# Kernel optimization log

Measured on AMD Instinct MI355X. Metric: run time of the kernel, lower is better.

The kernel has to match this reference:

```python
import jax, jax.numpy as jnp
import numpy as np

H = 12          # num_attention_heads
DH = 64         # attention_head_size (768/12)
LDH = 16        # layout head size (DH / channel_shrink_ratio=4)


def _split_heads(x, h, d):
    # [B,S,h*d] -> [B,h,S,d]
    B, S, _ = x.shape
    return x.reshape(B, S, h, d).transpose(0, 2, 1, 3)


def setup_inputs() -> dict:
    key = jax.random.key(0)
    ks = jax.random.split(key, 16)
    B, S, D, LD = 4, 2048, 768, 192
    std = 0.02
    inp = {
        "hidden_states": jax.random.normal(ks[0], (B, S, D), jnp.float32),
        "layout_hidden_states": jax.random.normal(ks[1], (B, S, LD), jnp.float32),
        "attention_mask": jnp.zeros((B, 1, 1, S), jnp.float32),
        # text-stream QKV (weights stored [in, out] so y = x @ W + b)
        "Wq": jax.random.normal(ks[2], (D, D), jnp.float32) * std,
        "bq": jnp.zeros((D,), jnp.float32),
        "Wk": jax.random.normal(ks[3], (D, D), jnp.float32) * std,
        "bk": jnp.zeros((D,), jnp.float32),
        "Wv": jax.random.normal(ks[4], (D, D), jnp.float32) * std,
        "bv": jnp.zeros((D,), jnp.float32),
        # layout-stream QKV
        "LWq": jax.random.normal(ks[5], (LD, LD), jnp.float32) * std,
        "Lbq": jnp.zeros((LD,), jnp.float32),
        "LWk": jax.random.normal(ks[6], (LD, LD), jnp.float32) * std,
        "Lbk": jnp.zeros((LD,), jnp.float32),
        "LWv": jax.random.normal(ks[7], (LD, LD), jnp.float32) * std,
        "Lbv": jnp.zeros((LD,), jnp.float32),
    }
    return inp


def reference(hidden_states, layout_hidden_states, attention_mask,
              Wq, bq, Wk, bk, Wv, bv, LWq, Lbq, LWk, Lbk, LWv, Lbv):
    B, S, D = hidden_states.shape
    LD = layout_hidden_states.shape[-1]

    q = _split_heads(hidden_states @ Wq + bq, H, DH)   # [B,H,S,DH]
    k = _split_heads(hidden_states @ Wk + bk, H, DH)
    v = _split_heads(hidden_states @ Wv + bv, H, DH)
    lq = _split_heads(layout_hidden_states @ LWq + Lbq, H, LDH)  # [B,H,S,LDH]
    lk = _split_heads(layout_hidden_states @ LWk + Lbk, H, LDH)
    lv = _split_heads(layout_hidden_states @ LWv + Lbv, H, LDH)

    # scaled per-stream scores
    scores_t = jnp.einsum('bhqd,bhkd->bhqk', q, k) / np.sqrt(DH).astype(np.float32)
    scores_l = jnp.einsum('bhqd,bhkd->bhqk', lq, lk) / np.sqrt(LDH).astype(np.float32)

    # bidirectional cross-addition (BiACM); layout branch detaches the text scores
    scores_text = scores_t + scores_l + attention_mask
    scores_layout = jax.lax.stop_gradient(scores_t) + scores_l + attention_mask

    probs_t = jax.nn.softmax(scores_text, axis=-1)
    probs_l = jax.nn.softmax(scores_layout, axis=-1)

    ctx = jnp.einsum('bhqk,bhkd->bhqd', probs_t, v)
    ctx = ctx.transpose(0, 2, 1, 3).reshape(B, S, H * DH)       # [B,S,768]
    lctx = jnp.einsum('bhqk,bhkd->bhqd', probs_l, lv)
    lctx = lctx.transpose(0, 2, 1, 3).reshape(B, S, H * LDH)    # [B,S,192]
    return (ctx, lctx)
```

## Files before the change

### kernel.cpp

```cpp
#include <hip/hip_runtime.h>
#include <hip/hip_bf16.h>
#include <cstdint>

typedef __attribute__((ext_vector_type(8))) short bf16x8;
typedef __attribute__((ext_vector_type(4))) float f32x4;

#define MFMA16(a, b, c) __builtin_amdgcn_mfma_f32_16x16x32_bf16((a), (b), (c), 0, 0, 0)

static __device__ __forceinline__ unsigned short f2b(float x) {
  __hip_bfloat16 h = __float2bfloat16(x);
  return __builtin_bit_cast(unsigned short, h);
}

__global__ __launch_bounds__(256) void cvt_f32_bf16(const float* __restrict__ s,
                                                    __hip_bfloat16* __restrict__ d, int n) {
  int stride = gridDim.x * 256 * 4;
  for (int i = (blockIdx.x * 256 + threadIdx.x) * 4; i < n; i += stride) {
    float4 v = *(const float4*)(s + i);
    ushort4 o;
    o.x = f2b(v.x); o.y = f2b(v.y); o.z = f2b(v.z); o.w = f2b(v.w);
    *(ushort4*)&d[i] = o;
  }
}

__global__ __launch_bounds__(256) void transpose_cvt(const float* __restrict__ s0,
                                                     const float* __restrict__ s1,
                                                     const float* __restrict__ s2,
                                                     __hip_bfloat16* __restrict__ dst,
                                                     int K, int N, int Npad) {
  __shared__ float tile[32][33];
  int p = blockIdx.z;
  const float* src = (p == 0) ? s0 : (p == 1) ? s1 : s2;
  int n0 = blockIdx.x * 32, k0 = blockIdx.y * 32;
  int tx = threadIdx.x & 31, ty = threadIdx.x >> 5;
  for (int i = ty; i < 32; i += 8) {
    int k = k0 + i, n = n0 + tx;
    tile[i][tx] = (k < K && n < N) ? src[(size_t)k * N + n] : 0.f;
  }
  __syncthreads();
  for (int i = ty; i < 32; i += 8) {
    int n = n0 + i, k = k0 + tx;
    if (n < Npad && k < K)
      dst[(size_t)p * Npad * K + (size_t)n * K + k] = __float2bfloat16(tile[tx][i]);
  }
}

template <int K, int N, int NPAD, int HD, int COFF>
__global__ __launch_bounds__(256, 2) void proj_gemm(
    const __hip_bfloat16* __restrict__ X, const __hip_bfloat16* __restrict__ Wt,
    const float* __restrict__ bq, const float* __restrict__ bk, const float* __restrict__ bv,
    __hip_bfloat16* __restrict__ qc, __hip_bfloat16* __restrict__ kc,
    __hip_bfloat16* __restrict__ vc, float qscale) {
  __shared__ __hip_bfloat16 lA[128 * 32];
  __shared__ __hip_bfloat16 lB[128 * 32];
  const int tid = threadIdx.x, w = tid >> 6, l = tid & 63;
  const int lr = l & 15, lg = l >> 4;
  const int p = blockIdx.z;
  const int m0 = blockIdx.x * 128, n0 = blockIdx.y * 128;
  const __hip_bfloat16* Wp = Wt + (size_t)p * NPAD * K;
  const float* bias = (p == 0) ? bq : (p == 1) ? bk : bv;
  const float scale = (p == 0) ? qscale : 1.0f;
  __hip_bfloat16* dstb = (p == 0) ? qc : (p == 1) ? kc : vc;

  f32x4 acc[4][4] = {};

  const int srow = (w * 2) * 16 + (l >> 2);
  const int scol = (l & 3) * 8;
  const __hip_bfloat16* gA = X + (size_t)(m0 + srow) * K + scol;
  const __hip_bfloat16* gB = Wp + (size_t)(n0 + srow) * K + scol;
  __hip_bfloat16* dA = lA + (w * 2) * 512;
  __hip_bfloat16* dB = lB + (w * 2) * 512;
  const int wr = w >> 1, wc = w & 1;

  for (int kk = 0; kk < K; kk += 32) {
    __builtin_amdgcn_global_load_lds((const __attribute__((address_space(1))) void*)(gA + kk),
                                     (__attribute__((address_space(3))) void*)dA, 16, 0, 0);
    __builtin_amdgcn_global_load_lds((const __attribute__((address_space(1))) void*)(gA + (size_t)16 * K + kk),
                                     (__attribute__((address_space(3))) void*)(dA + 512), 16, 0, 0);
    __builtin_amdgcn_global_load_lds((const __attribute__((address_space(1))) void*)(gB + kk),
                                     (__attribute__((address_space(3))) void*)dB, 16, 0, 0);
    __builtin_amdgcn_global_load_lds((const __attribute__((address_space(1))) void*)(gB + (size_t)16 * K + kk),
                                     (__attribute__((address_space(3))) void*)(dB + 512), 16, 0, 0);
    __syncthreads();
    bf16x8 af[4], bfr[4];
#pragma unroll
    for (int i = 0; i < 4; i++) af[i] = *(const bf16x8*)(lA + (wr * 64 + i * 16 + lr) * 32 + lg * 8);
#pragma unroll
    for (int j = 0; j < 4; j++) bfr[j] = *(const bf16x8*)(lB + (wc * 64 + j * 16 + lr) * 32 + lg * 8);
#pragma unroll
    for (int i = 0; i < 4; i++)
#pragma unroll
      for (int j = 0; j < 4; j++) acc[i][j] = MFMA16(bfr[j], af[i], acc[i][j]);
    __syncthreads();
  }

#pragma unroll
  for (int j = 0; j < 4; j++) {
    int nb = n0 + wc * 64 + j * 16 + lg * 4;
    if (NPAD > N && nb >= N) continue;
    float4 bv4 = *(const float4*)(bias + nb);
    int hh = nb / HD, d0 = nb % HD;
#pragma unroll
    for (int i = 0; i < 4; i++) {
      int m = m0 + wr * 64 + i * 16 + lr;
      int bb = m >> 11, s = m & 2047;
      size_t base = ((size_t)(bb * 12 + hh) * 2048 + s) * 80 + COFF + d0;
      ushort4 st;
      st.x = f2b((acc[i][j][0] + bv4.x) * scale);
      st.y = f2b((acc[i][j][1] + bv4.y) * scale);
      st.z = f2b((acc[i][j][2] + bv4.z) * scale);
      st.w = f2b((acc[i][j][3] + bv4.w) * scale);
      *(ushort4*)(dstb + base) = st;
    }
  }
}

__global__ __launch_bounds__(256) void transpose_v(const __hip_bfloat16* __restrict__ vc,
                                                   __hip_bfloat16* __restrict__ vt) {
  __shared__ __hip_bfloat16 t[32][34];
  int bh = blockIdx.z;
  int s0 = blockIdx.x * 32, d0 = blockIdx.y * 32;
  int tx = threadIdx.x & 31, ty = threadIdx.x >> 5;
  for (int i = ty; i < 32; i += 8) {
    int d = d0 + tx;
    if (d < 80) t[i][tx] = vc[((size_t)bh * 2048 + s0 + i) * 80 + d];
  }
  __syncthreads();
  for (int i = ty; i < 32; i += 8) {
    int d = d0 + i;
    if (d < 80) vt[((size_t)bh * 80 + d) * 2048 + s0 + tx] = t[tx][i];
  }
}

__global__ __launch_bounds__(256, 3) void attn_kernel(
    const __hip_bfloat16* __restrict__ qc, const __hip_bfloat16* __restrict__ kc,
    const __hip_bfloat16* __restrict__ vt, const float* __restrict__ mask,
    float* __restrict__ out, float* __restrict__ out2) {
  constexpr int KP = 88;
  constexpr int VP = 72;
  constexpr int SP = 72;
  __shared__ __hip_bfloat16 lK[64 * KP];
  __shared__ __hip_bfloat16 lV[96 * VP];
  __shared__ __hip_bfloat16 lP[4 * 32 * SP];
  const int tid = threadIdx.x, w = tid >> 6, l = tid & 63;
  const int lr = l & 15, lg = l >> 4;
  const int bh = blockIdx.y, b_ = bh / 12, h = bh - b_ * 12;
  const int q0 = blockIdx.x * 128;

  const __hip_bfloat16* gsrc[5];
  int gstep[5];
  __hip_bfloat16* ldst[5];
#pragma unroll
  for (int s = 0; s < 5; ++s) {
    int idx = tid + s * 256;
    if (idx < 640) {
      int r = idx / 10, c = idx - r * 10;
      gsrc[s] = kc + ((size_t)bh * 2048 + r) * 80 + c * 8;
      gstep[s] = 64 * 80;
      ldst[s] = lK + r * KP + c * 8;
    } else {
      int vi = idx - 640;
      int r = vi >> 3, c = vi & 7;
      gsrc[s] = vt + ((size_t)bh * 80 + r) * 2048 + c * 8;
      gstep[s] = 64;
      ldst[s] = lV + r * VP + c * 8;
    }
  }

  const bf16x8 zz = {0, 0, 0, 0, 0, 0, 0, 0};
  bf16x8 aq[2][3];
#pragma unroll
  for (int g = 0; g < 2; ++g) {
    const __hip_bfloat16* qrow = qc + ((size_t)bh * 2048 + q0 + w * 32 + g * 16 + lr) * 80;
    aq[g][0] = *(const bf16x8*)(qrow + lg * 8);
    aq[g][1] = *(const bf16x8*)(qrow + 32 + lg * 8);
    bf16x8 t = *(const bf16x8*)(qrow + 64 + (lg & 1) * 8);
    aq[g][2] = (lg < 2) ? t : zz;
  }

  if (tid < 128) {
    int r = 80 + (tid >> 3), c = tid & 7;
    short v = (r == 80) ? (short)0x3F80 : (short)0;
    bf16x8 x = {v, v, v, v, v, v, v, v};
    *(bf16x8*)(lV + r * VP + c * 8) = x;
  }
  {
    bf16x8 r0[5];
#pragma unroll
    for (int s = 0; s < 5; ++s) r0[s] = *(const bf16x8*)(gsrc[s]);
#pragma unroll
    for (int s = 0; s < 5; ++s) *(bf16x8*)(ldst[s]) = r0[s];
  }
  __syncthreads();

  float mrun[2][4];
#pragma unroll
  for (int g = 0; g < 2; ++g)
#pragma unroll
    for (int j = 0; j < 4; ++j) mrun[g][j] = -INFINITY;
  f32x4 o[2][6] = {};
  const float* maskb = mask + b_ * 2048;
  __hip_bfloat16* SPw = lP + w * 32 * SP;

  for (int kt = 0; kt < 32; ++kt) {
    int ktn = (kt + 1 < 32) ? kt + 1 : 31;
    bf16x8 pre[5];
#pragma unroll
    for (int s = 0; s < 5; ++s)
      pre[s] = *(const bf16x8*)(gsrc[s] + (size_t)ktn * gstep[s]);

    const int kv0 = kt * 64;
    float alpha[2][4];
#pragma unroll
    for (int g = 0; g < 2; ++g) {
      f32x4 sf[4] = {};
#pragma unroll
      for (int f = 0; f < 4; ++f) {
        const __hip_bfloat16* kr = lK + (f * 16 + lr) * KP;
        bf16x8 b0 = *(const bf16x8*)(kr + lg * 8);
        bf16x8 b1 = *(const bf16x8*)(kr + 32 + lg * 8);
        bf16x8 bt = *(const bf16x8*)(kr + 64 + (lg & 1) * 8);
        bf16x8 b2 = (lg < 2) ? bt : zz;
        sf[f] = MFMA16(aq[g][0], b0, sf[f]);
        sf[f] = MFMA16(aq[g][1], b1, sf[f]);
        sf[f] = MFMA16(aq[g][2], b2, sf[f]);
      }
#pragma unroll
      for (int f = 0; f < 4; ++f) {
        float mv = maskb[kv0 + f * 16 + lr];
#pragma unroll
        for (int j = 0; j < 4; ++j) sf[f][j] += mv;
      }
#pragma unroll
      for (int j = 0; j < 4; ++j) {
        float tm = fmaxf(fmaxf(sf[0][j], sf[1][j]), fmaxf(sf[2][j], sf[3][j]));
#pragma unroll
        for (int d = 1; d < 16; d <<= 1) tm = fmaxf(tm, __shfl_xor(tm, d));
        float nm = fmaxf(mrun[g][j], tm);
        alpha[g][j] = __expf(mrun[g][j] - nm);
        mrun[g][j] = nm;
#pragma unroll
        for (int f = 0; f < 4; ++f) sf[f][j] = __expf(sf[f][j] - nm);
      }
#pragma unroll
      for (int f = 0; f < 4; ++f)
#pragma unroll
        for (int j = 0; j < 4; ++j)
          SPw[(g * 16 + lg * 4 + j) * SP + f * 16 + lr] = __float2bfloat16(sf[f][j]);
    }
#pragma unroll
    for (int g = 0; g < 2; ++g)
#pragma unroll
      for (int c = 0; c < 6; ++c)
#pragma unroll
        for (int j = 0; j < 4; ++j) o[g][c][j] *= alpha[g][j];

#pragma unroll
    for (int t2 = 0; t2 < 2; ++t2) {
      bf16x8 pa0 = *(const bf16x8*)(SPw + lr * SP + t2 * 32 + lg * 8);
      bf16x8 pa1 = *(const bf16x8*)(SPw + (16 + lr) * SP + t2 * 32 + lg * 8);
#pragma unroll
      for (int c = 0; c < 6; ++c) {
        bf16x8 bv_ = *(const bf16x8*)(lV + (c * 16 + lr) * VP + t2 * 32 + lg * 8);
        o[0][c] = MFMA16(pa0, bv_, o[0][c]);
        o[1][c] = MFMA16(pa1, bv_, o[1][c]);
      }
    }
    __syncthreads();
#pragma unroll
    for (int s = 0; s < 5; ++s) *(bf16x8*)(ldst[s]) = pre[s];
    __syncthreads();
  }

#pragma unroll
  for (int g = 0; g < 2; ++g) {
#pragma unroll
    for (int j = 0; j < 4; ++j) {
      float den = __shfl(o[g][5][j], (l & 48));
      float inv = 1.0f / den;
      int qg = q0 + w * 32 + g * 16 + lg * 4 + j;
      float* ob = out + ((size_t)b_ * 2048 + qg) * 768 + h * 64;
#pragma unroll
      for (int c = 0; c < 4; ++c) ob[c * 16 + lr] = o[g][c][j] * inv;
      out2[((size_t)b_ * 2048 + qg) * 192 + h * 16 + lr] = o[g][4][j] * inv;
    }
  }
}

extern "C" void kernel_launch(void* const* d_in, const int* in_sizes, int n_in,
                              void* d_out, int out_size, void* d_ws, size_t ws_size,
                              hipStream_t stream) {
  const float* hidden = (const float*)d_in[0];
  const float* lhidden = (const float*)d_in[1];
  const float* mask = (const float*)d_in[2];
  const float* Wq = (const float*)d_in[3];
  const float* bq = (const float*)d_in[4];
  const float* Wk = (const float*)d_in[5];
  const float* bk = (const float*)d_in[6];
  const float* Wv = (const float*)d_in[7];
  const float* bv = (const float*)d_in[8];
  const float* LWq = (const float*)d_in[9];
  const float* Lbq = (const float*)d_in[10];
  const float* LWk = (const float*)d_in[11];
  const float* Lbk = (const float*)d_in[12];
  const float* LWv = (const float*)d_in[13];
  const float* Lbv = (const float*)d_in[14];

  char* ws = (char*)d_ws;
  __hip_bfloat16* Xb  = (__hip_bfloat16*)(ws + 0);
  __hip_bfloat16* LXb = (__hip_bfloat16*)(ws + 12582912);
  __hip_bfloat16* Wt  = (__hip_bfloat16*)(ws + 15728640);
  __hip_bfloat16* LWt = (__hip_bfloat16*)(ws + 19267584);
  __hip_bfloat16* qcb = (__hip_bfloat16*)(ws + 19562496);
  __hip_bfloat16* kcb = (__hip_bfloat16*)(ws + 35291136);
  __hip_bfloat16* vcb = (__hip_bfloat16*)(ws + 51019776);
  __hip_bfloat16* vtb = (__hip_bfloat16*)(ws + 66748416);

  float* out = (float*)d_out;
  float* out2 = out + (size_t)4 * 2048 * 768;

  cvt_f32_bf16<<<2048, 256, 0, stream>>>(hidden, Xb, 6291456);
  cvt_f32_bf16<<<1024, 256, 0, stream>>>(lhidden, LXb, 1572864);
  transpose_cvt<<<dim3(24, 24, 3), 256, 0, stream>>>(Wq, Wk, Wv, Wt, 768, 768, 768);
  transpose_cvt<<<dim3(8, 6, 3), 256, 0, stream>>>(LWq, LWk, LWv, LWt, 192, 192, 256);

  proj_gemm<768, 768, 768, 64, 0><<<dim3(64, 6, 3), 256, 0, stream>>>(
      Xb, Wt, bq, bk, bv, qcb, kcb, vcb, 0.125f);
  proj_gemm<192, 192, 256, 16, 64><<<dim3(64, 2, 3), 256, 0, stream>>>(
      LXb, LWt, Lbq, Lbk, Lbv, qcb, kcb, vcb, 0.25f);

  transpose_v<<<dim3(64, 3, 48), 256, 0, stream>>>(vcb, vtb);
  attn_kernel<<<dim3(16, 48), 256, 0, stream>>>(qcb, kcb, vtb, mask, out, out2);
}
```

Measured before the change: 338.0 us.

## Fuse V transpose into projection epilogue and streamline softmax with exp2 and lazy rescale

The projection GEMM now writes V directly in transposed [bh,d,s] layout, which removes the separate transpose_v kernel and its extra round trip through memory. The attention kernel swaps the MFMA operand order so each lane holds a full score row segment. This shortens the max reduction to two shuffles and allows vectorized mask loads and packed P stores. Scores are pre-scaled by log2(e) through the Q scale so exp2f can be used, and output rescaling is skipped unless the running max grows by more than 8. The transposed V stores are scalar and strided, which may be slow.

Result: faster. 319.7 us (-5.4%).

```diff
diff --git a/kernel.cpp b/kernel.cpp
--- a/kernel.cpp
+++ b/kernel.cpp
@@ -1,6 +1,7 @@
 #include <hip/hip_runtime.h>
 #include <hip/hip_bf16.h>
 #include <cstdint>
+#include <math.h>
 
 typedef __attribute__((ext_vector_type(8))) short bf16x8;
 typedef __attribute__((ext_vector_type(4))) float f32x4;
@@ -11,6 +12,8 @@
   __hip_bfloat16 h = __float2bfloat16(x);
   return __builtin_bit_cast(unsigned short, h);
 }
+
+#define INVLN2 1.4426950408889634f
 
 __global__ __launch_bounds__(256) void cvt_f32_bf16(const float* __restrict__ s,
                                                     __hip_bfloat16* __restrict__ d, int n) {
@@ -50,7 +53,7 @@
     const __hip_bfloat16* __restrict__ X, const __hip_bfloat16* __restrict__ Wt,
     const float* __restrict__ bq, const float* __restrict__ bk, const float* __restrict__ bv,
     __hip_bfloat16* __restrict__ qc, __hip_bfloat16* __restrict__ kc,
-    __hip_bfloat16* __restrict__ vc, float qscale) {
+    __hip_bfloat16* __restrict__ vt, float qscale) {
   __shared__ __hip_bfloat16 lA[128 * 32];
   __shared__ __hip_bfloat16 lB[128 * 32];
   const int tid = threadIdx.x, w = tid >> 6, l = tid & 63;
@@ -60,7 +63,6 @@
   const __hip_bfloat16* Wp = Wt + (size_t)p * NPAD * K;
   const float* bias = (p == 0) ? bq : (p == 1) ? bk : bv;
   const float scale = (p == 0) ? qscale : 1.0f;
-  __hip_bfloat16* dstb = (p == 0) ? qc : (p == 1) ? kc : vc;
 
   f32x4 acc[4][4] = {};
 
@@ -104,31 +106,22 @@
     for (int i = 0; i < 4; i++) {
       int m = m0 + wr * 64 + i * 16 + lr;
       int bb = m >> 11, s = m & 2047;
-      size_t base = ((size_t)(bb * 12 + hh) * 2048 + s) * 80 + COFF + d0;
-      ushort4 st;
-      st.x = f2b((acc[i][j][0] + bv4.x) * scale);
-      st.y = f2b((acc[i][j][1] + bv4.y) * scale);
-      st.z = f2b((acc[i][j][2] + bv4.z) * scale);
-      st.w = f2b((acc[i][j][3] + bv4.w) * scale);
-      *(ushort4*)(dstb + base) = st;
-    }
-  }
-}
-
-__global__ __launch_bounds__(256) void transpose_v(const __hip_bfloat16* __restrict__ vc,
-                                                   __hip_bfloat16* __restrict__ vt) {
-  __shared__ __hip_bfloat16 t[32][34];
-  int bh = blockIdx.z;
-  int s0 = blockIdx.x * 32, d0 = blockIdx.y * 32;
-  int tx = threadIdx.x & 31, ty = threadIdx.x >> 5;
-  for (int i = ty; i < 32; i += 8) {
-    int d = d0 + tx;
-    if (d < 80) t[i][tx] = vc[((size_t)bh * 2048 + s0 + i) * 80 + d];
-  }
-  __syncthreads();
-  for (int i = ty; i < 32; i += 8) {
-    int d = d0 + i;
-    if (d < 80) vt[((size_t)bh * 80 + d) * 2048 + s0 + tx] = t[tx][i];
+      if (p == 2) {
+        size_t based = ((size_t)(bb * 12 + hh) * 80 + COFF + d0) * 2048 + s;
+        vt[based]          = __float2bfloat16(acc[i][j][0] + bv4.x);
+        vt[based + 2048]   = __float2bfloat16(acc[i][j][1] + bv4.y);
+        vt[based + 4096]   = __float2bfloat16(acc[i][j][2] + bv4.z);
+        vt[based + 6144]   = __float2bfloat16(acc[i][j][3] + bv4.w);
+      } else {
+        size_t base = ((size_t)(bb * 12 + hh) * 2048 + s) * 80 + COFF + d0;
+        ushort4 st;
+        st.x = f2b((acc[i][j][0] + bv4.x) * scale);
+        st.y = f2b((acc[i][j][1] + bv4.y) * scale);
+        st.z = f2b((acc[i][j][2] + bv4.z) * scale);
+        st.w = f2b((acc[i][j][3] + bv4.w) * scale);
+        *(ushort4*)((p == 0 ? qc : kc) + base) = st;
+      }
+    }
   }
 }
 
@@ -193,11 +186,7 @@
   }
   __syncthreads();
 
-  float mrun[2][4];
-#pragma unroll
-  for (int g = 0; g < 2; ++g)
-#pragma unroll
-    for (int j = 0; j < 4; ++j) mrun[g][j] = -INFINITY;
+  float mrun[2] = {-INFINITY, -INFINITY};
   f32x4 o[2][6] = {};
   const float* maskb = mask + b_ * 2048;
   __hip_bfloat16* SPw = lP + w * 32 * SP;
@@ -210,50 +199,74 @@
       pre[s] = *(const bf16x8*)(gsrc[s] + (size_t)ktn * gstep[s]);
 
     const int kv0 = kt * 64;
-    float alpha[2][4];
+
+    f32x4 sf[2][4] = {};
+#pragma unroll
+    for (int f = 0; f < 4; ++f) {
+      const __hip_bfloat16* kr = lK + (f * 16 + lr) * KP;
+      bf16x8 b0 = *(const bf16x8*)(kr + lg * 8);
+      bf16x8 b1 = *(const bf16x8*)(kr + 32 + lg * 8);
+      bf16x8 bt = *(const bf16x8*)(kr + 64 + (lg & 1) * 8);
+      bf16x8 b2 = (lg < 2) ? bt : zz;
+#pragma unroll
+      for (int g = 0; g < 2; ++g) {
+        sf[g][f] = MFMA16(b0, aq[g][0], sf[g][f]);
+        sf[g][f] = MFMA16(b1, aq[g][1], sf[g][f]);
+        sf[g][f] = MFMA16(b2, aq[g][2], sf[g][f]);
+      }
+    }
+#pragma unroll
+    for (int f = 0; f < 4; ++f) {
+      float4 mv = *(const float4*)(maskb + kv0 + f * 16 + lg * 4);
+#pragma unroll
+      for (int g = 0; g < 2; ++g) {
+        sf[g][f][0] += mv.x * INVLN2;
+        sf[g][f][1] += mv.y * INVLN2;
+        sf[g][f][2] += mv.z * INVLN2;
+        sf[g][f][3] += mv.w * INVLN2;
+      }
+    }
+    float tm[2];
 #pragma unroll
     for (int g = 0; g < 2; ++g) {
-      f32x4 sf[4] = {};
+      float a01 = fmaxf(fmaxf(sf[g][0][0], sf[g][0][1]), fmaxf(sf[g][0][2], sf[g][0][3]));
+      float a23 = fmaxf(fmaxf(sf[g][1][0], sf[g][1][1]), fmaxf(sf[g][1][2], sf[g][1][3]));
+      float a45 = fmaxf(fmaxf(sf[g][2][0], sf[g][2][1]), fmaxf(sf[g][2][2], sf[g][2][3]));
+      float a67 = fmaxf(fmaxf(sf[g][3][0], sf[g][3][1]), fmaxf(sf[g][3][2], sf[g][3][3]));
+      float m = fmaxf(fmaxf(a01, a23), fmaxf(a45, a67));
+      m = fmaxf(m, __shfl_xor(m, 16));
+      m = fmaxf(m, __shfl_xor(m, 32));
+      tm[g] = m;
+    }
+    if (__any((tm[0] > mrun[0] + 8.f) || (tm[1] > mrun[1] + 8.f))) {
+      float nm0 = fmaxf(mrun[0], tm[0]), nm1 = fmaxf(mrun[1], tm[1]);
+      float a0 = exp2f(mrun[0] - nm0), a1 = exp2f(mrun[1] - nm1);
+      mrun[0] = nm0; mrun[1] = nm1;
+      float aO0[4], aO1[4];
+#pragma unroll
+      for (int j = 0; j < 4; ++j) {
+        aO0[j] = __shfl(a0, lg * 4 + j);
+        aO1[j] = __shfl(a1, lg * 4 + j);
+      }
+#pragma unroll
+      for (int c = 0; c < 6; ++c)
+#pragma unroll
+        for (int j = 0; j < 4; ++j) {
+          o[0][c][j] *= aO0[j];
+          o[1][c][j] *= aO1[j];
+        }
+    }
+#pragma unroll
+    for (int g = 0; g < 2; ++g)
 #pragma unroll
       for (int f = 0; f < 4; ++f) {
-        const __hip_bfloat16* kr = lK + (f * 16 + lr) * KP;
-        bf16x8 b0 = *(const bf16x8*)(kr + lg * 8);
-        bf16x8 b1 = *(const bf16x8*)(kr + 32 + lg * 8);
-        bf16x8 bt = *(const bf16x8*)(kr + 64 + (lg & 1) * 8);
-        bf16x8 b2 = (lg < 2) ? bt : zz;
-        sf[f] = MFMA16(aq[g][0], b0, sf[f]);
-        sf[f] = MFMA16(aq[g][1], b1, sf[f]);
-        sf[f] = MFMA16(aq[g][2], b2, sf[f]);
-      }
-#pragma unroll
-      for (int f = 0; f < 4; ++f) {
-        float mv = maskb[kv0 + f * 16 + lr];
-#pragma unroll
-        for (int j = 0; j < 4; ++j) sf[f][j] += mv;
-      }
-#pragma unroll
-      for (int j = 0; j < 4; ++j) {
-        float tm = fmaxf(fmaxf(sf[0][j], sf[1][j]), fmaxf(sf[2][j], sf[3][j]));
-#pragma unroll
-        for (int d = 1; d < 16; d <<= 1) tm = fmaxf(tm, __shfl_xor(tm, d));
-        float nm = fmaxf(mrun[g][j], tm);
-        alpha[g][j] = __expf(mrun[g][j] - nm);
-        mrun[g][j] = nm;
-#pragma unroll
-        for (int f = 0; f < 4; ++f) sf[f][j] = __expf(sf[f][j] - nm);
-      }
-#pragma unroll
-      for (int f = 0; f < 4; ++f)
-#pragma unroll
-        for (int j = 0; j < 4; ++j)
-          SPw[(g * 16 + lg * 4 + j) * SP + f * 16 + lr] = __float2bfloat16(sf[f][j]);
-    }
-#pragma unroll
-    for (int g = 0; g < 2; ++g)
-#pragma unroll
-      for (int c = 0; c < 6; ++c)
-#pragma unroll
-        for (int j = 0; j < 4; ++j) o[g][c][j] *= alpha[g][j];
+        ushort4 pk;
+        pk.x = f2b(exp2f(sf[g][f][0] - mrun[g]));
+        pk.y = f2b(exp2f(sf[g][f][1] - mrun[g]));
+        pk.z = f2b(exp2f(sf[g][f][2] - mrun[g]));
+        pk.w = f2b(exp2f(sf[g][f][3] - mrun[g]));
+        *(ushort4*)(SPw + (g * 16 + lr) * SP + f * 16 + lg * 4) = pk;
+      }
 
 #pragma unroll
     for (int t2 = 0; t2 < 2; ++t2) {
@@ -313,8 +326,7 @@
   __hip_bfloat16* LWt = (__hip_bfloat16*)(ws + 19267584);
   __hip_bfloat16* qcb = (__hip_bfloat16*)(ws + 19562496);
   __hip_bfloat16* kcb = (__hip_bfloat16*)(ws + 35291136);
-  __hip_bfloat16* vcb = (__hip_bfloat16*)(ws + 51019776);
-  __hip_bfloat16* vtb = (__hip_bfloat16*)(ws + 66748416);
+  __hip_bfloat16* vtb = (__hip_bfloat16*)(ws + 51019776);
 
   float* out = (float*)d_out;
   float* out2 = out + (size_t)4 * 2048 * 768;
@@ -325,10 +337,9 @@
   transpose_cvt<<<dim3(8, 6, 3), 256, 0, stream>>>(LWq, LWk, LWv, LWt, 192, 192, 256);
 
   proj_gemm<768, 768, 768, 64, 0><<<dim3(64, 6, 3), 256, 0, stream>>>(
-      Xb, Wt, bq, bk, bv, qcb, kcb, vcb, 0.125f);
+      Xb, Wt, bq, bk, bv, qcb, kcb, vtb, 0.125f * INVLN2);
   proj_gemm<192, 192, 256, 16, 64><<<dim3(64, 2, 3), 256, 0, stream>>>(
-      LXb, LWt, Lbq, Lbk, Lbv, qcb, kcb, vcb, 0.25f);
-
-  transpose_v<<<dim3(64, 3, 48), 256, 0, stream>>>(vcb, vtb);
+      LXb, LWt, Lbq, Lbk, Lbv, qcb, kcb, vtb, 0.25f * INVLN2);
+
   attn_kernel<<<dim3(16, 48), 256, 0, stream>>>(qcb, kcb, vtb, mask, out, out2);
 }
```
